# Kernel tuning notes

Hardware: AMD Instinct MI355X
Metric: run time of the kernel (lower is better)

## Reference

```python
import jax, jax.numpy as jnp
import numpy as np

D_MODEL = 1024
NUM_HEADS = 16
D_K = D_MODEL // NUM_HEADS
B, S = 4, 2048
NEG_INF = -1.0e9  # matches torch masked_fill value


def setup_inputs() -> dict:
    key = jax.random.key(0)
    ks = jax.random.split(key, 6)
    scale = 1.0 / np.sqrt(D_MODEL)
    x = jax.random.normal(ks[0], (B, S, D_MODEL), dtype=jnp.float32)
    # causal mask, broadcast over batch and heads: [1,1,S,S]
    mask = jnp.tril(jnp.ones((S, S), dtype=jnp.int32))[None, None]
    Wq = jax.random.normal(ks[1], (D_MODEL, D_MODEL), dtype=jnp.float32) * scale
    Wk = jax.random.normal(ks[2], (D_MODEL, D_MODEL), dtype=jnp.float32) * scale
    Wv = jax.random.normal(ks[3], (D_MODEL, D_MODEL), dtype=jnp.float32) * scale
    Wo = jax.random.normal(ks[4], (D_MODEL, D_MODEL), dtype=jnp.float32) * scale
    bq = jnp.zeros((D_MODEL,), jnp.float32)
    bk = jnp.zeros((D_MODEL,), jnp.float32)
    bv = jnp.zeros((D_MODEL,), jnp.float32)
    bo = jnp.zeros((D_MODEL,), jnp.float32)
    return {"x": x, "mask": mask, "Wq": Wq, "bq": bq, "Wk": Wk, "bk": bk,
            "Wv": Wv, "bv": bv, "Wo": Wo, "bo": bo}


def reference(x, mask, Wq, bq, Wk, bk, Wv, bv, Wo, bo):
    b, s, d = x.shape
    # projections (torch Linear: y = x @ W.T + b)
    q = (x @ Wq.T + bq).reshape(b, s, NUM_HEADS, D_K).transpose(0, 2, 1, 3)  # [B,H,S,Dk]
    k = (x @ Wk.T + bk).reshape(b, s, NUM_HEADS, D_K).transpose(0, 2, 1, 3)
    v = (x @ Wv.T + bv).reshape(b, s, NUM_HEADS, D_K).transpose(0, 2, 1, 3)
    scores = jnp.einsum("bhqd,bhkd->bhqk", q, k) / jnp.sqrt(jnp.float32(D_K))
    scores = jnp.where(mask == 0, NEG_INF, scores)
    attn = jax.nn.softmax(scores, axis=-1)
    out = jnp.einsum("bhqk,bhkd->bhqd", attn, v)  # [B,H,S,Dk]
    out = out.transpose(0, 2, 1, 3).reshape(b, s, d)
    return out @ Wo.T + bo
```

## Files before the change

### kernel.cpp

```cpp
#include <hip/hip_runtime.h>
#include <hip/hip_bf16.h>

#define D_MODEL 1024
#define NUM_HEADS 16
#define DK 64
#define BATCH 4
#define SEQ 2048

typedef __hip_bfloat16 bf16;
typedef __attribute__((ext_vector_type(8))) short bf16x8;
typedef __attribute__((ext_vector_type(4))) short bf16x4;
typedef __attribute__((ext_vector_type(4))) float f32x4;

typedef __attribute__((address_space(1))) const unsigned int gu32;
typedef __attribute__((address_space(3))) unsigned int lu32;

#define QSCALE (0.125f * 1.44269504089f)

#define FENCE asm volatile("" ::: "memory")
#define BAR_OPEN()  do { FENCE; __builtin_amdgcn_s_barrier();              \
    asm volatile("s_waitcnt lgkmcnt(0)" ::: "memory");                     \
    __builtin_amdgcn_sched_barrier(0); } while (0)
#define BAR_CLOSE() do { FENCE; __builtin_amdgcn_s_barrier(); FENCE; } while (0)

__device__ __forceinline__ void gll16(const bf16* g, bf16* l) {
    __builtin_amdgcn_global_load_lds((gu32*)g, (lu32*)l, 16, 0, 0);
}

__device__ __forceinline__ bf16x8 frag_ld(const bf16* lds, int row, int h, int quad) {
    return *(const bf16x8*)(lds + row * 64 + (((h << 2) + quad) ^ (row & 7)) * 8);
}

__global__ __launch_bounds__(256)
void cvt_bf16(const float* __restrict__ x,  const float* __restrict__ Wq,
              const float* __restrict__ Wk, const float* __restrict__ Wv,
              const float* __restrict__ Wo, bf16* __restrict__ xb,
              bf16* __restrict__ Wb)
{
    size_t v = (size_t)blockIdx.x * 256 + threadIdx.x;
    size_t e = v * 4;
    const float* src; bf16* dst; size_t off;
    if (e < 8388608) { src = x; dst = xb; off = e; }
    else {
        size_t r = e - 8388608;
        int w = (int)(r >> 20);
        off = r & 1048575;
        src = (w == 0) ? Wq : (w == 1) ? Wk : (w == 2) ? Wv : Wo;
        dst = Wb + ((size_t)w << 20);
    }
    float4 f = *(const float4*)(src + off);
    bf16 o[4] = {__float2bfloat16(f.x), __float2bfloat16(f.y),
                 __float2bfloat16(f.z), __float2bfloat16(f.w)};
    *(bf16x4*)(dst + off) = *(const bf16x4*)o;
}

__global__ __launch_bounds__(512, 1)
void gemm_qkv(const bf16* __restrict__ A, const bf16* __restrict__ W,
              const float* __restrict__ bqv, const float* __restrict__ bkv,
              const float* __restrict__ bvv,
              bf16* __restrict__ Q, bf16* __restrict__ Kt, bf16* __restrict__ Vtr)
{
    __shared__ bf16 lds[65536];

    const int t = threadIdx.x;
    const int wave = t >> 6, lane = t & 63;
    const int quad = lane >> 4, l16 = lane & 15;
    const int wm = wave >> 2, wn = wave & 3;

    const int colb = blockIdx.x;
    const int rowBase = blockIdx.y * 256;

    const bf16* Ablk = A + (size_t)rowBase * 1024;
    const bf16* Bblk = W + (size_t)colb * 256 * 1024;

    auto stageAhalf = [&](int d, int h, int k0) {
        bf16* dst = (bf16*)lds + d * 16384 + h * 8192;
        #pragma unroll
        for (int p = 0; p < 2; ++p) {
            int idx = t + p * 512;
            int row = idx >> 3, cg = (idx & 7) ^ (row & 7);
            gll16(Ablk + (size_t)(h * 128 + row) * 1024 + k0 + cg * 8, dst + idx * 8);
        }
    };
    auto stageBhalf = [&](int d, int h, int k0) {
        bf16* dst = (bf16*)lds + 32768 + d * 16384 + h * 8192;
        #pragma unroll
        for (int p = 0; p < 2; ++p) {
            int idx = t + p * 512;
            int row = idx >> 3, cg = (idx & 7) ^ (row & 7);
            gll16(Bblk + (size_t)(h * 128 + row) * 1024 + k0 + cg * 8, dst + idx * 8);
        }
    };

    f32x4 acc[8][4];
    #pragma unroll
    for (int mf = 0; mf < 8; ++mf)
        #pragma unroll
        for (int nf = 0; nf < 4; ++nf) acc[mf][nf] = (f32x4){0.f, 0.f, 0.f, 0.f};

    const bf16* Aha = (const bf16*)lds + wm * 8192;
    const bf16* Ahb = (const bf16*)lds + 16384 + wm * 8192;
    const bf16* Bha = (const bf16*)lds + 32768 + (wn >> 1) * 8192;
    const bf16* Bhb = (const bf16*)lds + 49152 + (wn >> 1) * 8192;
    const int brow0 = (wn & 1) * 64;

    auto rdA4 = [&](bf16x8 (&f)[4][2], const bf16* Ah, int mh) {
        #pragma unroll
        for (int m4 = 0; m4 < 4; ++m4)
            #pragma unroll
            for (int kk = 0; kk < 2; ++kk)
                f[m4][kk] = frag_ld(Ah, mh * 64 + m4 * 16 + l16, kk, quad);
    };
    auto rdB2 = [&](bf16x8 (&f)[2][2], const bf16* Bh, int nh) {
        #pragma unroll
        for (int n2 = 0; n2 < 2; ++n2)
            #pragma unroll
            for (int kk = 0; kk < 2; ++kk)
                f[n2][kk] = frag_ld(Bh, brow0 + nh * 32 + n2 * 16 + l16, kk, quad);
    };
    auto mfma16 = [&](bf16x8 (&af)[4][2], bf16x8 (&bfr)[2][2], int mh, int nh) {
        __builtin_amdgcn_s_setprio(1);
        #pragma unroll
        for (int kk = 0; kk < 2; ++kk)
            #pragma unroll
            for (int m4 = 0; m4 < 4; ++m4)
                #pragma unroll
                for (int n2 = 0; n2 < 2; ++n2)
                    acc[mh * 4 + m4][nh * 2 + n2] =
                        __builtin_amdgcn_mfma_f32_16x16x32_bf16(
                            af[m4][kk], bfr[n2][kk], acc[mh * 4 + m4][nh * 2 + n2],
                            0, 0, 0);
        __builtin_amdgcn_s_setprio(0);
    };

    stageBhalf(0, 0, 0);  stageBhalf(0, 1, 0);
    stageAhalf(0, 0, 0);  stageAhalf(0, 1, 0);
    stageBhalf(1, 0, 64); stageBhalf(1, 1, 64);
    stageAhalf(1, 0, 64); stageAhalf(1, 1, 64);
    asm volatile("s_waitcnt vmcnt(8)" ::: "memory");
    FENCE; __builtin_amdgcn_s_barrier(); FENCE;

    for (int it = 0; it < 8; ++it) {
        const bool more = (it < 7);
        const int ka2 = it * 128 + 128, kb2 = ka2 + 64;
        bf16x8 aX[4][2], aY[4][2], bX[2][2], bY[2][2];

        rdA4(aX, Aha, 0); rdB2(bX, Bha, 0);
        asm volatile("s_waitcnt lgkmcnt(8)" ::: "memory");
        BAR_OPEN(); mfma16(aX, bX, 0, 0); BAR_CLOSE();

        rdB2(bY, Bha, 1);
        BAR_OPEN(); mfma16(aX, bY, 0, 1); BAR_CLOSE();

        rdA4(aY, Aha, 1);
        if (more) stageBhalf(0, 0, ka2);
        BAR_OPEN(); mfma16(aY, bY, 1, 1); BAR_CLOSE();

        if (more) stageBhalf(0, 1, ka2);
        BAR_OPEN(); mfma16(aY, bX, 1, 0);
        if (more) asm volatile("s_waitcnt vmcnt(4)" ::: "memory");
        else      asm volatile("s_waitcnt vmcnt(0)" ::: "memory");
        BAR_CLOSE();

        rdA4(aX, Ahb, 0); rdB2(bX, Bhb, 0);
        if (more) stageAhalf(0, 0, ka2);
        asm volatile("s_waitcnt lgkmcnt(8)" ::: "memory");
        BAR_OPEN(); mfma16(aX, bX, 0, 0); BAR_CLOSE();

        rdB2(bY, Bhb, 1);
        if (more) stageAhalf(0, 1, ka2);
        BAR_OPEN(); mfma16(aX, bY, 0, 1); BAR_CLOSE();

        rdA4(aY, Ahb, 1);
        if (more) { stageBhalf(1, 0, kb2); stageBhalf(1, 1, kb2); }
        BAR_OPEN(); mfma16(aY, bY, 1, 1); BAR_CLOSE();

        if (more) { stageAhalf(1, 0, kb2); stageAhalf(1, 1, kb2); }
        BAR_OPEN(); mfma16(aY, bX, 1, 0);
        if (more) {
            asm volatile("s_waitcnt vmcnt(8)" ::: "memory");
            BAR_CLOSE();
        }
    }

    {
        const int proj = colb >> 2;
        const float* bias = proj == 0 ? bqv : (proj == 1 ? bkv : bvv);
        const int cb = (colb & 3) * 256;
        float bias4[4];
        #pragma unroll
        for (int nf = 0; nf < 4; ++nf)
            bias4[nf] = bias[cb + wn * 64 + nf * 16 + l16];
        const float oscale = proj == 0 ? QSCALE : 1.0f;
        #pragma unroll
        for (int mf = 0; mf < 8; ++mf)
            #pragma unroll
            for (int rr = 0; rr < 4; ++rr) {
                int r = rowBase + wm * 128 + mf * 16 + quad * 4 + rr;
                int b_ = r >> 11, s_ = r & 2047;
                #pragma unroll
                for (int nf = 0; nf < 4; ++nf) {
                    int c = cb + wn * 64 + nf * 16 + l16;
                    float v = (acc[mf][nf][rr] + bias4[nf]) * oscale;
                    int h_ = c >> 6, d_ = c & 63;
                    size_t bh = (size_t)(b_ * NUM_HEADS + h_);
                    if (proj == 2)
                        Vtr[(bh * DK + d_) * SEQ + s_] = __float2bfloat16(v);
                    else {
                        bf16* dst = proj == 0 ? Q : Kt;
                        dst[(bh * SEQ + s_) * DK + d_] = __float2bfloat16(v);
                    }
                }
            }
    }
}

__device__ __forceinline__ void stage_gll128(const bf16* __restrict__ src,
                                             bf16* lds, int t, int k0)
{
    #pragma unroll
    for (int p = 0; p < 4; ++p) {
        int idx = t + p * 256;
        int row = idx >> 3, cl = idx & 7;
        int cg = cl ^ (row & 7);
        gll16(src + (size_t)row * 1024 + k0 + cg * 8, lds + idx * 8);
    }
}

__global__ __launch_bounds__(256)
void gemm_out(const bf16* __restrict__ ctx, const bf16* __restrict__ Wb,
              const float* __restrict__ bo, float* __restrict__ out)
{
    __shared__ bf16 As[128 * 64];
    __shared__ bf16 Bs[128 * 64];
    const int t = threadIdx.x;
    const int wave = t >> 6, lane = t & 63;
    const int quad = lane >> 4, l16 = lane & 15;
    const int wr = wave >> 1, wc = wave & 1;
    const int colBase = blockIdx.x * 128;
    const int rowBase = blockIdx.y * 128;

    const bf16* Ablk = ctx + (size_t)rowBase * 1024;
    const bf16* Bblk = Wb + ((size_t)3 << 20) + (size_t)colBase * 1024;

    f32x4 acc[4][4];
    #pragma unroll
    for (int i = 0; i < 4; ++i)
        #pragma unroll
        for (int j = 0; j < 4; ++j) acc[i][j] = (f32x4){0.f, 0.f, 0.f, 0.f};

    for (int k0 = 0; k0 < 1024; k0 += 64) {
        stage_gll128(Ablk, As, t, k0);
        stage_gll128(Bblk, Bs, t, k0);
        __syncthreads();
        #pragma unroll
        for (int h = 0; h < 2; ++h) {
            bf16x8 af[4], bfr[4];
            #pragma unroll
            for (int i = 0; i < 4; ++i)
                af[i] = frag_ld(As, wr * 64 + i * 16 + l16, h, quad);
            #pragma unroll
            for (int j = 0; j < 4; ++j)
                bfr[j] = frag_ld(Bs, wc * 64 + j * 16 + l16, h, quad);
            #pragma unroll
            for (int i = 0; i < 4; ++i)
                #pragma unroll
                for (int j = 0; j < 4; ++j)
                    acc[i][j] = __builtin_amdgcn_mfma_f32_16x16x32_bf16(af[i], bfr[j],
                                                                        acc[i][j], 0, 0, 0);
        }
        __syncthreads();
    }

    float bias4[4];
    #pragma unroll
    for (int j = 0; j < 4; ++j)
        bias4[j] = bo[colBase + wc * 64 + j * 16 + l16];

    #pragma unroll
    for (int i = 0; i < 4; ++i)
        #pragma unroll
        for (int rr = 0; rr < 4; ++rr) {
            int r = rowBase + wr * 64 + i * 16 + quad * 4 + rr;
            #pragma unroll
            for (int j = 0; j < 4; ++j) {
                int c = colBase + wc * 64 + j * 16 + l16;
                out[(size_t)r * 1024 + c] = acc[i][j][rr] + bias4[j];
            }
        }
}

#define AS 72

__device__ __forceinline__ void stage_attn(const bf16* __restrict__ Kb,
                                           const bf16* __restrict__ Vb,
                                           int k0, bf16* ks, bf16* vs, int t)
{
    #pragma unroll
    for (int p = 0; p < 2; ++p) {
        int idx = t + p * 256;
        int row = idx >> 3, cl = idx & 7;
        int cg = cl ^ (row & 7);
        gll16(Kb + (size_t)(k0 + row) * DK + cg * 8, ks + idx * 8);
        gll16(Vb + (size_t)row * SEQ + k0 + cg * 8, vs + idx * 8);
    }
}

__global__ __launch_bounds__(256)
void attn_mfma(const bf16* __restrict__ Q, const bf16* __restrict__ K,
               const bf16* __restrict__ Vt, bf16* __restrict__ ctx)
{
    __shared__ bf16 Ks[2][64 * 64];
    __shared__ bf16 Vs[2][64 * 64];
    __shared__ bf16 Ps[4][2][16 * AS];

    const int t    = threadIdx.x;
    const int wave = t >> 6, lane = t & 63;
    const int quad = lane >> 4, l16 = lane & 15;
    const int bh   = blockIdx.x;
    const int qbi  = 15 - blockIdx.y;
    const int b_ = bh >> 4, h_ = bh & 15;

    const bf16* Qb = Q  + (size_t)bh * SEQ * DK;
    const bf16* Kb = K  + (size_t)bh * SEQ * DK;
    const bf16* Vb = Vt + (size_t)bh * DK * SEQ;

    const int qb  = qbi * 128;
    const int ntiles = 2 * qbi + 2;

    bf16x8 qf[2][2];
    #pragma unroll
    for (int i = 0; i < 2; ++i) {
        const int qrow = qb + wave * 32 + i * 16 + l16;
        qf[i][0] = *(const bf16x8*)(Qb + (size_t)qrow * DK + quad * 8);
        qf[i][1] = *(const bf16x8*)(Qb + (size_t)qrow * DK + 32 + quad * 8);
    }

    f32x4 O[2][4];
    float lsum[2][4];
    #pragma unroll
    for (int i = 0; i < 2; ++i)
        #pragma unroll
        for (int nc = 0; nc < 4; ++nc) {
            O[i][nc] = (f32x4){0.f, 0.f, 0.f, 0.f};
            lsum[i][nc] = 0.f;
        }

    stage_attn(Kb, Vb, 0, Ks[0], Vs[0], t);
    __syncthreads();

    for (int kt = 0; kt < ntiles; ++kt) {
        const int cur = kt & 1;
        const int k0  = kt * 64;
        if (kt + 1 < ntiles)
            stage_attn(Kb, Vb, k0 + 64, Ks[cur ^ 1], Vs[cur ^ 1], t);

        const bool diag = (kt + 2 >= ntiles);
        const bool skip = (kt == ntiles - 1) && (wave < 2);

        if (!skip) {
            bf16x8 kf[4][2];
            #pragma unroll
            for (int h = 0; h < 4; ++h) {
                kf[h][0] = frag_ld(Ks[cur], h * 16 + l16, 0, quad);
                kf[h][1] = frag_ld(Ks[cur], h * 16 + l16, 1, quad);
            }

            #pragma unroll
            for (int i = 0; i < 2; ++i) {
                const int qrow0i = qb + wave * 32 + i * 16;
                float lacc[4];
                #pragma unroll
                for (int r = 0; r < 4; ++r) lacc[r] = lsum[i][r];
                #pragma unroll
                for (int h = 0; h < 4; ++h) {
                    f32x4 a = (f32x4){0.f, 0.f, 0.f, 0.f};
                    a = __builtin_amdgcn_mfma_f32_16x16x32_bf16(qf[i][0], kf[h][0], a, 0, 0, 0);
                    a = __builtin_amdgcn_mfma_f32_16x16x32_bf16(qf[i][1], kf[h][1], a, 0, 0, 0);
                    #pragma unroll
                    for (int r = 0; r < 4; ++r) {
                        float ss = a[r];
                        if (diag && (k0 + h * 16 + l16 > qrow0i + quad * 4 + r))
                            ss = -1e30f;
                        float p = exp2f(ss);
                        lacc[r] += p;
                        Ps[wave][i][(quad * 4 + r) * AS + h * 16 + l16] =
                            __float2bfloat16(p);
                    }
                }
                #pragma unroll
                for (int r = 0; r < 4; ++r) lsum[i][r] = lacc[r];
            }

            bf16x8 pf[2][2];
            #pragma unroll
            for (int i = 0; i < 2; ++i) {
                pf[i][0] = *(const bf16x8*)(&Ps[wave][i][l16 * AS + quad * 8]);
                pf[i][1] = *(const bf16x8*)(&Ps[wave][i][l16 * AS + 32 + quad * 8]);
            }
            __builtin_amdgcn_s_setprio(1);
            #pragma unroll
            for (int nc = 0; nc < 4; ++nc) {
                bf16x8 vf0 = frag_ld(Vs[cur], nc * 16 + l16, 0, quad);
                bf16x8 vf1 = frag_ld(Vs[cur], nc * 16 + l16, 1, quad);
                #pragma unroll
                for (int i = 0; i < 2; ++i) {
                    O[i][nc] = __builtin_amdgcn_mfma_f32_16x16x32_bf16(pf[i][0], vf0, O[i][nc], 0, 0, 0);
                    O[i][nc] = __builtin_amdgcn_mfma_f32_16x16x32_bf16(pf[i][1], vf1, O[i][nc], 0, 0, 0);
                }
            }
            __builtin_amdgcn_s_setprio(0);
        }
        __syncthreads();
    }

    #pragma unroll
    for (int i = 0; i < 2; ++i) {
        float inv[4];
        #pragma unroll
        for (int r = 0; r < 4; ++r) {
            #pragma unroll
            for (int off = 1; off < 16; off <<= 1)
                lsum[i][r] += __shfl_xor(lsum[i][r], off, 64);
            inv[r] = __builtin_amdgcn_rcpf(lsum[i][r]);
        }
        #pragma unroll
        for (int nc = 0; nc < 4; ++nc)
            #pragma unroll
            for (int r = 0; r < 4; ++r) {
                const int row = qb + wave * 32 + i * 16 + quad * 4 + r;
                float v = O[i][nc][r] * inv[r];
                ctx[((size_t)(b_ * SEQ + row)) * D_MODEL + h_ * DK + nc * 16 + l16] =
                    __float2bfloat16(v);
            }
    }
}

extern "C" void kernel_launch(void* const* d_in, const int* in_sizes, int n_in,
                              void* d_out, int out_size, void* d_ws, size_t ws_size,
                              hipStream_t stream) {
    const float* x  = (const float*)d_in[0];
    const float* Wq = (const float*)d_in[2];
    const float* bq = (const float*)d_in[3];
    const float* Wk = (const float*)d_in[4];
    const float* bk = (const float*)d_in[5];
    const float* Wv = (const float*)d_in[6];
    const float* bv = (const float*)d_in[7];
    const float* Wo = (const float*)d_in[8];
    const float* bo = (const float*)d_in[9];
    float* out = (float*)d_out;

    const size_t per = (size_t)BATCH * NUM_HEADS * SEQ * DK;
    bf16* Q   = (bf16*)d_ws;
    bf16* Kt  = Q  + per;
    bf16* Vtr = Kt + per;
    bf16* xb  = Vtr + per;
    bf16* ctx = xb;
    bf16* Wb  = xb + per;

    hipLaunchKernelGGL(cvt_bf16, dim3(12288), dim3(256), 0, stream,
                       x, Wq, Wk, Wv, Wo, xb, Wb);

    hipLaunchKernelGGL(gemm_qkv, dim3(12, 32), dim3(512), 0, stream,
                       xb, Wb, bq, bk, bv, Q, Kt, Vtr);

    hipLaunchKernelGGL(attn_mfma, dim3(64, 16), dim3(256), 0,
                       stream, Q, Kt, Vtr, ctx);

    hipLaunchKernelGGL(gemm_out, dim3(8, 64), dim3(256), 0, stream,
                       ctx, Wb, bo, out);
}
```

Measured before the change: 299.9 us.

## Keep softmax probabilities in registers via transposed QK^T and bpermute

The attention kernel now computes S^T (K as the A operand), so each lane holds probabilities for one query row. It packs them to bf16 and redistributes them into the PV MFMA A-operand layout with ds_bpermute, which removes the per-wave LDS round trip for P. Off-diagonal tiles are peeled into a separate loop with no causal-mask logic, and row sums become one scalar per lane, finished with cross-quad shuffles and a bpermute transpose. In exchange it adds many bpermute operations per tile and more complex code.

```diff
diff --git a/kernel.cpp b/kernel.cpp
--- a/kernel.cpp
+++ b/kernel.cpp
@@ -30,6 +30,16 @@
 __device__ __forceinline__ bf16x8 frag_ld(const bf16* lds, int row, int h, int quad) {
     return *(const bf16x8*)(lds + row * 64 + (((h << 2) + quad) ^ (row & 7)) * 8);
 }
+
+__device__ __forceinline__ unsigned int pack2(float lo, float hi) {
+    bf16 l = __float2bfloat16(lo), h = __float2bfloat16(hi);
+    unsigned short lu, hu;
+    __builtin_memcpy(&lu, &l, 2);
+    __builtin_memcpy(&hu, &h, 2);
+    return ((unsigned int)hu << 16) | lu;
+}
+
+typedef union { bf16x8 v; unsigned int u[4]; } frag_u;
 
 __global__ __launch_bounds__(256)
 void cvt_bf16(const float* __restrict__ x,  const float* __restrict__ Wq,
@@ -290,8 +300,6 @@
         }
 }
 
-#define AS 72
-
 __device__ __forceinline__ void stage_attn(const bf16* __restrict__ Kb,
                                            const bf16* __restrict__ Vb,
                                            int k0, bf16* ks, bf16* vs, int t)
@@ -312,7 +320,6 @@
 {
     __shared__ bf16 Ks[2][64 * 64];
     __shared__ bf16 Vs[2][64 * 64];
-    __shared__ bf16 Ps[4][2][16 * AS];
 
     const int t    = threadIdx.x;
     const int wave = t >> 6, lane = t & 63;
@@ -328,6 +335,9 @@
     const int qb  = qbi * 128;
     const int ntiles = 2 * qbi + 2;
 
+    const int addrA = ((2 * (quad & 1)) * 16 + l16) * 4;
+    const int addrB = ((2 * (quad & 1) + 1) * 16 + l16) * 4;
+
     bf16x8 qf[2][2];
     #pragma unroll
     for (int i = 0; i < 2; ++i) {
@@ -337,25 +347,82 @@
     }
 
     f32x4 O[2][4];
-    float lsum[2][4];
+    float lsum[2] = {0.f, 0.f};
     #pragma unroll
     for (int i = 0; i < 2; ++i)
         #pragma unroll
-        for (int nc = 0; nc < 4; ++nc) {
-            O[i][nc] = (f32x4){0.f, 0.f, 0.f, 0.f};
-            lsum[i][nc] = 0.f;
-        }
+        for (int nc = 0; nc < 4; ++nc) O[i][nc] = (f32x4){0.f, 0.f, 0.f, 0.f};
 
     stage_attn(Kb, Vb, 0, Ks[0], Vs[0], t);
     __syncthreads();
 
-    for (int kt = 0; kt < ntiles; ++kt) {
+    auto pv_window = [&](unsigned int (&pk)[2][2][2], int hp, const bf16* Vsc) {
+        bf16x8 pa[2];
+        #pragma unroll
+        for (int i = 0; i < 2; ++i) {
+            frag_u fa;
+            #pragma unroll
+            for (int j2 = 0; j2 < 4; ++j2) {
+                const int ad = (j2 >> 1) ? addrB : addrA;
+                int lo = __builtin_amdgcn_ds_bpermute(ad, (int)pk[i][0][j2 & 1]);
+                int hi = __builtin_amdgcn_ds_bpermute(ad, (int)pk[i][1][j2 & 1]);
+                fa.u[j2] = (quad >> 1) ? (unsigned int)hi : (unsigned int)lo;
+            }
+            pa[i] = fa.v;
+        }
+        __builtin_amdgcn_s_setprio(1);
+        #pragma unroll
+        for (int nc = 0; nc < 4; ++nc) {
+            bf16x8 vf = frag_ld(Vsc, nc * 16 + l16, hp, quad);
+            #pragma unroll
+            for (int i = 0; i < 2; ++i)
+                O[i][nc] = __builtin_amdgcn_mfma_f32_16x16x32_bf16(pa[i], vf, O[i][nc], 0, 0, 0);
+        }
+        __builtin_amdgcn_s_setprio(0);
+    };
+
+    int kt = 0;
+
+    for (; kt < ntiles - 2; ++kt) {
+        const int cur = kt & 1;
+        stage_attn(Kb, Vb, kt * 64 + 64, Ks[cur ^ 1], Vs[cur ^ 1], t);
+
+        bf16x8 kf[4][2];
+        #pragma unroll
+        for (int h = 0; h < 4; ++h) {
+            kf[h][0] = frag_ld(Ks[cur], h * 16 + l16, 0, quad);
+            kf[h][1] = frag_ld(Ks[cur], h * 16 + l16, 1, quad);
+        }
+
+        #pragma unroll
+        for (int hp = 0; hp < 2; ++hp) {
+            unsigned int pk[2][2][2];
+            #pragma unroll
+            for (int hh = 0; hh < 2; ++hh) {
+                const int h = hp * 2 + hh;
+                #pragma unroll
+                for (int i = 0; i < 2; ++i) {
+                    f32x4 a = (f32x4){0.f, 0.f, 0.f, 0.f};
+                    a = __builtin_amdgcn_mfma_f32_16x16x32_bf16(kf[h][0], qf[i][0], a, 0, 0, 0);
+                    a = __builtin_amdgcn_mfma_f32_16x16x32_bf16(kf[h][1], qf[i][1], a, 0, 0, 0);
+                    float p0 = exp2f(a[0]), p1 = exp2f(a[1]);
+                    float p2 = exp2f(a[2]), p3 = exp2f(a[3]);
+                    lsum[i] += (p0 + p1) + (p2 + p3);
+                    pk[i][hh][0] = pack2(p0, p1);
+                    pk[i][hh][1] = pack2(p2, p3);
+                }
+            }
+            pv_window(pk, hp, Vs[cur]);
+        }
+        __syncthreads();
+    }
+
+    for (; kt < ntiles; ++kt) {
         const int cur = kt & 1;
         const int k0  = kt * 64;
         if (kt + 1 < ntiles)
             stage_attn(Kb, Vb, k0 + 64, Ks[cur ^ 1], Vs[cur ^ 1], t);
 
-        const bool diag = (kt + 2 >= ntiles);
         const bool skip = (kt == ntiles - 1) && (wave < 2);
 
         if (!skip) {
@@ -367,62 +434,45 @@
             }
 
             #pragma unroll
-            for (int i = 0; i < 2; ++i) {
-                const int qrow0i = qb + wave * 32 + i * 16;
-                float lacc[4];
+            for (int hp = 0; hp < 2; ++hp) {
+                unsigned int pk[2][2][2];
                 #pragma unroll
-                for (int r = 0; r < 4; ++r) lacc[r] = lsum[i][r];
-                #pragma unroll
-                for (int h = 0; h < 4; ++h) {
-                    f32x4 a = (f32x4){0.f, 0.f, 0.f, 0.f};
-                    a = __builtin_amdgcn_mfma_f32_16x16x32_bf16(qf[i][0], kf[h][0], a, 0, 0, 0);
-                    a = __builtin_amdgcn_mfma_f32_16x16x32_bf16(qf[i][1], kf[h][1], a, 0, 0, 0);
+                for (int hh = 0; hh < 2; ++hh) {
+                    const int h = hp * 2 + hh;
                     #pragma unroll
-                    for (int r = 0; r < 4; ++r) {
-                        float ss = a[r];
-                        if (diag && (k0 + h * 16 + l16 > qrow0i + quad * 4 + r))
-                            ss = -1e30f;
-                        float p = exp2f(ss);
-                        lacc[r] += p;
-                        Ps[wave][i][(quad * 4 + r) * AS + h * 16 + l16] =
-                            __float2bfloat16(p);
+                    for (int i = 0; i < 2; ++i) {
+                        const int qrow = qb + wave * 32 + i * 16 + l16;
+                        f32x4 a = (f32x4){0.f, 0.f, 0.f, 0.f};
+                        a = __builtin_amdgcn_mfma_f32_16x16x32_bf16(kf[h][0], qf[i][0], a, 0, 0, 0);
+                        a = __builtin_amdgcn_mfma_f32_16x16x32_bf16(kf[h][1], qf[i][1], a, 0, 0, 0);
+                        float p[4];
+                        #pragma unroll
+                        for (int r = 0; r < 4; ++r) {
+                            float ss = a[r];
+                            if (k0 + h * 16 + quad * 4 + r > qrow) ss = -1e30f;
+                            p[r] = exp2f(ss);
+                        }
+                        lsum[i] += (p[0] + p[1]) + (p[2] + p[3]);
+                        pk[i][hh][0] = pack2(p[0], p[1]);
+                        pk[i][hh][1] = pack2(p[2], p[3]);
                     }
                 }
-                #pragma unroll
-                for (int r = 0; r < 4; ++r) lsum[i][r] = lacc[r];
-            }
-
-            bf16x8 pf[2][2];
-            #pragma unroll
-            for (int i = 0; i < 2; ++i) {
-                pf[i][0] = *(const bf16x8*)(&Ps[wave][i][l16 * AS + quad * 8]);
-                pf[i][1] = *(const bf16x8*)(&Ps[wave][i][l16 * AS + 32 + quad * 8]);
-            }
-            __builtin_amdgcn_s_setprio(1);
-            #pragma unroll
-            for (int nc = 0; nc < 4; ++nc) {
-                bf16x8 vf0 = frag_ld(Vs[cur], nc * 16 + l16, 0, quad);
-                bf16x8 vf1 = frag_ld(Vs[cur], nc * 16 + l16, 1, quad);
-                #pragma unroll
-                for (int i = 0; i < 2; ++i) {
-                    O[i][nc] = __builtin_amdgcn_mfma_f32_16x16x32_bf16(pf[i][0], vf0, O[i][nc], 0, 0, 0);
-                    O[i][nc] = __builtin_amdgcn_mfma_f32_16x16x32_bf16(pf[i][1], vf1, O[i][nc], 0, 0, 0);
-                }
-            }
-            __builtin_amdgcn_s_setprio(0);
+                pv_window(pk, hp, Vs[cur]);
+            }
         }
         __syncthreads();
     }
 
     #pragma unroll
     for (int i = 0; i < 2; ++i) {
+        lsum[i] += __shfl_xor(lsum[i], 16, 64);
+        lsum[i] += __shfl_xor(lsum[i], 32, 64);
         float inv[4];
         #pragma unroll
         for (int r = 0; r < 4; ++r) {
-            #pragma unroll
-            for (int off = 1; off < 16; off <<= 1)
-                lsum[i][r] += __shfl_xor(lsum[i][r], off, 64);
-            inv[r] = __builtin_amdgcn_rcpf(lsum[i][r]);
+            float tot = __int_as_float(__builtin_amdgcn_ds_bpermute(
+                (quad * 20 + r) * 4, __float_as_int(lsum[i])));
+            inv[r] = __builtin_amdgcn_rcpf(tot);
         }
         #pragma unroll
         for (int nc = 0; nc < 4; ++nc)
```

Result: no change. 301.8 us (+0.6%).
